# Performance work log

Measured on AMD Instinct MI355X. Metric: run time of the kernel, lower is better.

## Reference

```python
import jax, jax.numpy as jnp
import numpy as np


def setup_inputs() -> dict:
    key = jax.random.key(0)
    ks = jax.random.split(key, 8)
    B, L, C = 128, 196, 2048  # batch, locations (att_size^2), channels
    H, D = 512, 1024          # att_hid_size, decoder hidden_size
    return {
        "att_features": jax.random.normal(ks[0], (B, L, C), dtype=jnp.float32),
        "h": jax.random.normal(ks[1], (B, D), dtype=jnp.float32),
        "Wc": jax.random.normal(ks[2], (L, H), dtype=jnp.float32) * 0.05,
        "bc": jax.random.normal(ks[3], (H,), dtype=jnp.float32) * 0.05,
        "Wh": jax.random.normal(ks[4], (D, H), dtype=jnp.float32) * 0.05,
        "bh": jax.random.normal(ks[5], (H,), dtype=jnp.float32) * 0.05,
        "wa": jax.random.normal(ks[6], (H,), dtype=jnp.float32) * 0.05,
        "ba": jnp.zeros((1,), dtype=jnp.float32),
    }


def reference(att_features, h, Wc, bc, Wh, bh, wa, ba):
    B, L, C = att_features.shape
    # reshape to (B, locations, C) then permute -> (B, C, locations)
    x = jnp.transpose(att_features.reshape(B, L, C), (0, 2, 1))  # (B, C, L)
    ca = jnp.einsum('bcl,lh->bch', x, Wc) + bc                   # channel2att: (B, C, H)
    ph = h @ Wh + bh                                              # h2att: (B, H)
    # alpha_net(tanh(broadcast add)) -> (B, C)
    scores = jnp.einsum('bch,h->bc', jnp.tanh(ca + ph[:, None, :]), wa) + ba[0]
    weights = jax.nn.softmax(scores, axis=1)                      # softmax over channels
    # bmm: (B,1,C) @ (B,C,L) -> (B, L)
    weighted = jnp.einsum('bc,bcl->bl', weights, x)
    return weighted, weights
```

## Files before the change

### kernel.cpp

```cpp
#include <hip/hip_runtime.h>

#define B_   128
#define L_   196
#define C_   2048
#define H_   512
#define D_   1024
#define KP   224
#define CT   256
#define NITER 14

#define SMEM_BYTES (131072 + 4096)

typedef __bf16 bf16x8 __attribute__((ext_vector_type(8)));
typedef float  f32x2  __attribute__((ext_vector_type(2)));
typedef float  f32x4  __attribute__((ext_vector_type(4)));

__device__ __forceinline__ int permc(int c) { return ((c >> 2) & 7) ^ ((c & 2) << 1); }

__global__ __launch_bounds__(256) void k_wc3(const float* __restrict__ Wc, __bf16* __restrict__ wcb3) {
    int grp = blockIdx.x * 256 + threadIdx.x;
    int m  = grp & 15;
    int g  = (grp >> 4) & 3;
    int rb = (grp >> 6) & 31;
    int kk = grp >> 11;
    int h  = rb * 16 + m;
    bf16x8 v;
#pragma unroll
    for (int j = 0; j < 8; ++j) {
        int k = kk * 32 + g * 8 + j;
        v[j] = (k < L_) ? (__bf16)Wc[(size_t)k * H_ + h] : (__bf16)0.0f;
    }
    *(bf16x8*)&wcb3[(size_t)grp * 8] = v;
}

__global__ __launch_bounds__(512) void k_ph(const float* __restrict__ h, const float* __restrict__ Wh,
                                            const float* __restrict__ bh, const float* __restrict__ bc,
                                            float* __restrict__ ph_ws) {
    int b0 = blockIdx.x * 4;
    int t = threadIdx.x;
    __shared__ float hs[4][D_];
    for (int idx = t; idx < 4 * D_; idx += 512)
        hs[idx >> 10][idx & (D_ - 1)] = h[(size_t)(b0 + (idx >> 10)) * D_ + (idx & (D_ - 1))];
    __syncthreads();
    float base = bh[t] + bc[t];
    float a0 = base, a1 = base, a2 = base, a3 = base;
#pragma unroll 8
    for (int d = 0; d < D_; ++d) {
        float wv = Wh[(size_t)d * H_ + t];
        a0 += hs[0][d] * wv; a1 += hs[1][d] * wv; a2 += hs[2][d] * wv; a3 += hs[3][d] * wv;
    }
    ph_ws[(size_t)(b0 + 0) * H_ + t] = a0;
    ph_ws[(size_t)(b0 + 1) * H_ + t] = a1;
    ph_ws[(size_t)(b0 + 2) * H_ + t] = a2;
    ph_ws[(size_t)(b0 + 3) * H_ + t] = a3;
}

__device__ __forceinline__ float fast_tanh(float x) {
    x = fminf(fmaxf(x, -15.f), 15.f);
    float e = __builtin_amdgcn_exp2f(x * 2.8853900817779268f);
    return 1.0f - 2.0f * __builtin_amdgcn_rcpf(e + 1.0f);
}

__global__ __launch_bounds__(512, 2) void k_scores(const float* __restrict__ att, const __bf16* __restrict__ wcb3,
                                                   const float* __restrict__ ph_ws, const float* __restrict__ wa,
                                                   const float* __restrict__ ba, float* __restrict__ scores) {
    extern __shared__ char smem[];
    __bf16* att_s = (__bf16*)smem;
    float*  sred  = (float*)(smem + 131072);

    const int t = threadIdx.x, lane = t & 63, wid = t >> 6;
    const int wm = wid >> 1, wn = wid & 1;
    const int ct = blockIdx.x, b = blockIdx.y;
    const float* attb = att + ((size_t)b * L_) * C_ + ct * CT;

    const int cpr = t & 127, sl = t >> 7;
    const int c0s = cpr * 2;
    const int pmS = permc(c0s);

    const int n_ = lane & 15, g_ = lane >> 4;
    const int crow0 = wn * 128 + n_;
    const int t2 = (n_ & 2) << 1;
    const int qb = crow0 >> 2;

    f32x2 sv[8];
    auto STAGE_LOAD = [&](int kk) {
#pragma unroll
        for (int j = 0; j < 8; ++j) {
            int l = kk * 32 + sl * 8 + j;
            if (l < L_) sv[j] = *(const f32x2*)(attb + (size_t)l * C_ + c0s);
            else { sv[j][0] = 0.f; sv[j][1] = 0.f; }
        }
    };
    auto STAGE_WRITE = [&](int kk) {
        int p = (kk * 4 + sl) ^ pmS;
        bf16x8 r0, r1;
#pragma unroll
        for (int j = 0; j < 8; ++j) { r0[j] = (__bf16)sv[j][0]; r1[j] = (__bf16)sv[j][1]; }
        *(bf16x8*)&att_s[c0s * 256 + p * 8] = r0;
        *(bf16x8*)&att_s[(c0s + 1) * 256 + p * 8] = r1;
    };

    bf16x8 afr[4], afrN[4];
    const __bf16* apA = wcb3 + (size_t)lane * 8;
    auto ALOAD = [&](int it, bf16x8* dst) {
        int hc = (it >= 7) ? 1 : 0;
        int kk = it - hc * 7;
#pragma unroll
        for (int mf = 0; mf < 4; ++mf) {
            int rb = hc * 16 + wm * 4 + mf;
            dst[mf] = *(const bf16x8*)(apA + (size_t)(kk * 32 + rb) * 512);
        }
    };

    ALOAD(0, afr);
    STAGE_LOAD(0);
    STAGE_WRITE(0);
    __syncthreads();

    f32x4 zero4 = {0.f, 0.f, 0.f, 0.f};
    f32x4 acc[4][8];
#pragma unroll
    for (int mf = 0; mf < 4; ++mf)
#pragma unroll
        for (int nf = 0; nf < 8; ++nf) acc[mf][nf] = zero4;
    float spart[8] = {0.f, 0.f, 0.f, 0.f, 0.f, 0.f, 0.f, 0.f};

    for (int it = 0; it < NITER; ++it) {
        const int hc = (it >= 7) ? 1 : 0;
        const int kk = it - hc * 7;

        if (it + 1 < NITER) ALOAD(it + 1, afrN);
        if (it < 6) STAGE_LOAD(it + 1);

        bf16x8 bfr[8];
        const int sb = kk * 4 + g_;
#pragma unroll
        for (int nf = 0; nf < 8; ++nf) {
            int p = sb ^ (((qb + nf * 4) & 7) ^ t2);
            bfr[nf] = *(const bf16x8*)&att_s[(crow0 + nf * 16) * 256 + p * 8];
        }
#pragma unroll
        for (int mf = 0; mf < 4; ++mf)
#pragma unroll
            for (int nf = 0; nf < 8; ++nf)
                acc[mf][nf] = __builtin_amdgcn_mfma_f32_16x16x32_bf16(afr[mf], bfr[nf], acc[mf][nf], 0, 0, 0);

        if (it < 6) STAGE_WRITE(it + 1);

        if (kk == 6) {
            const int rbase = hc * 256 + wm * 64 + g_ * 4;
#pragma unroll
            for (int mf = 0; mf < 4; ++mf) {
                const int row = rbase + mf * 16;
                f32x4 phv = *(const f32x4*)&ph_ws[(size_t)b * H_ + row];
                f32x4 wav = *(const f32x4*)&wa[row];
#pragma unroll
                for (int nf = 0; nf < 8; ++nf) {
                    f32x4 tv = acc[mf][nf];
                    float ss = 0.f;
#pragma unroll
                    for (int r = 0; r < 4; ++r)
                        ss += fast_tanh(tv[r] + phv[r]) * wav[r];
                    spart[nf] += ss;
                    acc[mf][nf] = zero4;
                }
            }
        }

        if (it < 6) __syncthreads();

        if (it + 1 < NITER) {
#pragma unroll
            for (int mf = 0; mf < 4; ++mf) afr[mf] = afrN[mf];
        }
    }

#pragma unroll
    for (int nf = 0; nf < 8; ++nf) {
        spart[nf] += __shfl_xor(spart[nf], 16);
        spart[nf] += __shfl_xor(spart[nf], 32);
    }
    if (g_ == 0) {
#pragma unroll
        for (int nf = 0; nf < 8; ++nf) sred[(wid * 8 + nf) * 16 + n_] = spart[nf];
    }
    __syncthreads();
    if (wid < 2 && g_ == 0) {
        const float ba0 = ba[0];
#pragma unroll
        for (int nf = 0; nf < 8; ++nf) {
            float v = ba0;
#pragma unroll
            for (int wmm = 0; wmm < 4; ++wmm) v += sred[((wmm * 2 + wid) * 8 + nf) * 16 + n_];
            scores[(size_t)b * C_ + ct * CT + wid * 128 + nf * 16 + n_] = v;
        }
    }
}

__global__ __launch_bounds__(512) void k_fused(const float* __restrict__ att, const float* __restrict__ sc,
                                               float* __restrict__ out) {
    __shared__ float w_s[C_];
    __shared__ float red[8], red2[8];
    const int b = blockIdx.y, q = blockIdx.x;
    const int t = threadIdx.x;
    const int lane = t & 63, wid = t >> 6;

    const float* sp = sc + (size_t)b * C_;
    float v[4];
#pragma unroll
    for (int j = 0; j < 4; ++j) v[j] = sp[j * 512 + t];
    float m = fmaxf(fmaxf(v[0], v[1]), fmaxf(v[2], v[3]));
#pragma unroll
    for (int off = 32; off >= 1; off >>= 1) m = fmaxf(m, __shfl_xor(m, off));
    if (lane == 0) red[wid] = m;
    __syncthreads();
#pragma unroll
    for (int w = 0; w < 8; ++w) m = fmaxf(m, red[w]);
    float s = 0.f;
#pragma unroll
    for (int j = 0; j < 4; ++j) {
        v[j] = __builtin_amdgcn_exp2f((v[j] - m) * 1.4426950408889634f);
        s += v[j];
    }
#pragma unroll
    for (int off = 32; off >= 1; off >>= 1) s += __shfl_xor(s, off);
    if (lane == 0) red2[wid] = s;
    __syncthreads();
    s = 0.f;
#pragma unroll
    for (int w = 0; w < 8; ++w) s += red2[w];
    float inv = 1.0f / s;
    float* wout = out + B_ * L_;
#pragma unroll
    for (int j = 0; j < 4; ++j) {
        float wv = v[j] * inv;
        w_s[j * 512 + t] = wv;
        if (q == 0) wout[(size_t)b * C_ + j * 512 + t] = wv;
    }
    __syncthreads();

    for (int l = wid; l < 49; l += 8) {
        int gl = q * 49 + l;
        const float* ap = att + ((size_t)b * L_ + gl) * C_;
        float acc = 0.f;
#pragma unroll
        for (int j = 0; j < 8; ++j) {
            int c = j * 256 + lane * 4;
            f32x4 a4 = *(const f32x4*)(ap + c);
            f32x4 w4 = *(const f32x4*)&w_s[c];
            acc += a4[0] * w4[0] + a4[1] * w4[1] + a4[2] * w4[2] + a4[3] * w4[3];
        }
#pragma unroll
        for (int off = 32; off >= 1; off >>= 1) acc += __shfl_xor(acc, off);
        if (lane == 0) out[(size_t)b * L_ + gl] = acc;
    }
}

extern "C" void kernel_launch(void* const* d_in, const int* in_sizes, int n_in,
                              void* d_out, int out_size, void* d_ws, size_t ws_size,
                              hipStream_t stream) {
    const float* att = (const float*)d_in[0];
    const float* h   = (const float*)d_in[1];
    const float* Wc  = (const float*)d_in[2];
    const float* bc  = (const float*)d_in[3];
    const float* Wh  = (const float*)d_in[4];
    const float* bh  = (const float*)d_in[5];
    const float* wa  = (const float*)d_in[6];
    const float* ba  = (const float*)d_in[7];
    float* out = (float*)d_out;

    float* ph_ws  = (float*)d_ws;
    float* scores = ph_ws + B_ * H_;
    __bf16* wcb3  = (__bf16*)(scores + (size_t)B_ * C_);

    hipFuncSetAttribute((const void*)k_scores, hipFuncAttributeMaxDynamicSharedMemorySize, SMEM_BYTES);

    k_wc3   <<<dim3(56), 256, 0, stream>>>(Wc, wcb3);
    k_ph    <<<dim3(B_ / 4), 512, 0, stream>>>(h, Wh, bh, bc, ph_ws);
    k_scores<<<dim3(C_ / CT, B_), 512, SMEM_BYTES, stream>>>(att, wcb3, ph_ws, wa, ba, scores);
    k_fused <<<dim3(4, B_), 512, 0, stream>>>(att, scores, out);
}
```

Baseline: 454.8 us.

## Halve score tile width, pad LDS rows, merge prep kernels, dual-row weighted sum

The channel tile of the scores kernel drops from 256 to 128 with a padded row stride of 224 bf16 instead of a 256-wide XOR permutation, so LDS use shrinks and launch bounds allow four blocks per CU. The A-fragment double buffer is replaced by loading the next fragments after the MFMAs, the loop is fully unrolled with setprio around the MFMA section, and barriers become a lighter lgkmcnt wait plus s_barrier. The Wc conversion and h2att kernels are merged into one launch, fast_tanh loses its clamp, and the weighted-sum kernel handles two locations per wave iteration for more memory-level parallelism. The narrower tile halves B-fragment reuse per A load and doubles the grid, and without the clamp very large arguments rely on exp2 saturating to inf.

```diff
diff --git a/kernel.cpp b/kernel.cpp
--- a/kernel.cpp
+++ b/kernel.cpp
@@ -5,146 +5,138 @@
 #define C_   2048
 #define H_   512
 #define D_   1024
-#define KP   224
-#define CT   256
+#define CT   128
 #define NITER 14
-
-#define SMEM_BYTES (131072 + 4096)
+#define RSE  224
 
 typedef __bf16 bf16x8 __attribute__((ext_vector_type(8)));
-typedef float  f32x2  __attribute__((ext_vector_type(2)));
 typedef float  f32x4  __attribute__((ext_vector_type(4)));
 
-__device__ __forceinline__ int permc(int c) { return ((c >> 2) & 7) ^ ((c & 2) << 1); }
-
-__global__ __launch_bounds__(256) void k_wc3(const float* __restrict__ Wc, __bf16* __restrict__ wcb3) {
-    int grp = blockIdx.x * 256 + threadIdx.x;
-    int m  = grp & 15;
-    int g  = (grp >> 4) & 3;
-    int rb = (grp >> 6) & 31;
-    int kk = grp >> 11;
-    int h  = rb * 16 + m;
-    bf16x8 v;
-#pragma unroll
-    for (int j = 0; j < 8; ++j) {
-        int k = kk * 32 + g * 8 + j;
-        v[j] = (k < L_) ? (__bf16)Wc[(size_t)k * H_ + h] : (__bf16)0.0f;
-    }
-    *(bf16x8*)&wcb3[(size_t)grp * 8] = v;
-}
-
-__global__ __launch_bounds__(512) void k_ph(const float* __restrict__ h, const float* __restrict__ Wh,
-                                            const float* __restrict__ bh, const float* __restrict__ bc,
-                                            float* __restrict__ ph_ws) {
-    int b0 = blockIdx.x * 4;
-    int t = threadIdx.x;
+__global__ __launch_bounds__(512) void k_prep(const float* __restrict__ Wc, __bf16* __restrict__ wcb3,
+                                              const float* __restrict__ h, const float* __restrict__ Wh,
+                                              const float* __restrict__ bh, const float* __restrict__ bc,
+                                              float* __restrict__ ph_ws) {
     __shared__ float hs[4][D_];
-    for (int idx = t; idx < 4 * D_; idx += 512)
-        hs[idx >> 10][idx & (D_ - 1)] = h[(size_t)(b0 + (idx >> 10)) * D_ + (idx & (D_ - 1))];
-    __syncthreads();
-    float base = bh[t] + bc[t];
-    float a0 = base, a1 = base, a2 = base, a3 = base;
+    const int bid = blockIdx.x, t = threadIdx.x;
+    if (bid < 28) {
+        int grp = bid * 512 + t;
+        int m  = grp & 15;
+        int g  = (grp >> 4) & 3;
+        int rb = (grp >> 6) & 31;
+        int kk = grp >> 11;
+        int hh = rb * 16 + m;
+        bf16x8 v;
+#pragma unroll
+        for (int j = 0; j < 8; ++j) {
+            int k = kk * 32 + g * 8 + j;
+            v[j] = (k < L_) ? (__bf16)Wc[(size_t)k * H_ + hh] : (__bf16)0.0f;
+        }
+        *(bf16x8*)&wcb3[(size_t)grp * 8] = v;
+    } else {
+        int b0 = (bid - 28) * 4;
+        for (int idx = t; idx < 4 * D_; idx += 512)
+            hs[idx >> 10][idx & (D_ - 1)] = h[(size_t)(b0 + (idx >> 10)) * D_ + (idx & (D_ - 1))];
+        __syncthreads();
+        float base = bh[t] + bc[t];
+        float a0 = base, a1 = base, a2 = base, a3 = base;
 #pragma unroll 8
-    for (int d = 0; d < D_; ++d) {
-        float wv = Wh[(size_t)d * H_ + t];
-        a0 += hs[0][d] * wv; a1 += hs[1][d] * wv; a2 += hs[2][d] * wv; a3 += hs[3][d] * wv;
-    }
-    ph_ws[(size_t)(b0 + 0) * H_ + t] = a0;
-    ph_ws[(size_t)(b0 + 1) * H_ + t] = a1;
-    ph_ws[(size_t)(b0 + 2) * H_ + t] = a2;
-    ph_ws[(size_t)(b0 + 3) * H_ + t] = a3;
+        for (int d = 0; d < D_; ++d) {
+            float wv = Wh[(size_t)d * H_ + t];
+            a0 += hs[0][d] * wv; a1 += hs[1][d] * wv; a2 += hs[2][d] * wv; a3 += hs[3][d] * wv;
+        }
+        ph_ws[(size_t)(b0 + 0) * H_ + t] = a0;
+        ph_ws[(size_t)(b0 + 1) * H_ + t] = a1;
+        ph_ws[(size_t)(b0 + 2) * H_ + t] = a2;
+        ph_ws[(size_t)(b0 + 3) * H_ + t] = a3;
+    }
 }
 
 __device__ __forceinline__ float fast_tanh(float x) {
-    x = fminf(fmaxf(x, -15.f), 15.f);
     float e = __builtin_amdgcn_exp2f(x * 2.8853900817779268f);
-    return 1.0f - 2.0f * __builtin_amdgcn_rcpf(e + 1.0f);
-}
-
-__global__ __launch_bounds__(512, 2) void k_scores(const float* __restrict__ att, const __bf16* __restrict__ wcb3,
+    return fmaf(-2.0f, __builtin_amdgcn_rcpf(e + 1.0f), 1.0f);
+}
+
+__device__ __forceinline__ void block_sync_lds() {
+    asm volatile("s_waitcnt lgkmcnt(0)" ::: "memory");
+    __builtin_amdgcn_sched_barrier(0);
+    __builtin_amdgcn_s_barrier();
+    __builtin_amdgcn_sched_barrier(0);
+}
+
+__global__ __launch_bounds__(512, 4) void k_scores(const float* __restrict__ att, const __bf16* __restrict__ wcb3,
                                                    const float* __restrict__ ph_ws, const float* __restrict__ wa,
                                                    const float* __restrict__ ba, float* __restrict__ scores) {
-    extern __shared__ char smem[];
-    __bf16* att_s = (__bf16*)smem;
-    float*  sred  = (float*)(smem + 131072);
+    __shared__ __bf16 att_s[CT * RSE];
+    __shared__ float  sred[8][4][16];
 
     const int t = threadIdx.x, lane = t & 63, wid = t >> 6;
     const int wm = wid >> 1, wn = wid & 1;
     const int ct = blockIdx.x, b = blockIdx.y;
     const float* attb = att + ((size_t)b * L_) * C_ + ct * CT;
 
-    const int cpr = t & 127, sl = t >> 7;
-    const int c0s = cpr * 2;
-    const int pmS = permc(c0s);
+    const int sc = t & 127, sl = t >> 7;
+    const int spdst = sc * RSE + (sl ^ ((sc >> 1) & 3)) * 8;
 
     const int n_ = lane & 15, g_ = lane >> 4;
-    const int crow0 = wn * 128 + n_;
-    const int t2 = (n_ & 2) << 1;
-    const int qb = crow0 >> 2;
-
-    f32x2 sv[8];
+    const int bbase = (wn * 64 + n_) * RSE + (g_ ^ ((n_ >> 1) & 3)) * 8;
+
+    const __bf16* apA = wcb3 + (size_t)lane * 8;
+
+    float sv[8];
+    bf16x8 afr[4];
+
     auto STAGE_LOAD = [&](int kk) {
 #pragma unroll
         for (int j = 0; j < 8; ++j) {
             int l = kk * 32 + sl * 8 + j;
-            if (l < L_) sv[j] = *(const f32x2*)(attb + (size_t)l * C_ + c0s);
-            else { sv[j][0] = 0.f; sv[j][1] = 0.f; }
+            sv[j] = (l < L_) ? attb[(size_t)l * C_ + sc] : 0.0f;
         }
     };
     auto STAGE_WRITE = [&](int kk) {
-        int p = (kk * 4 + sl) ^ pmS;
-        bf16x8 r0, r1;
-#pragma unroll
-        for (int j = 0; j < 8; ++j) { r0[j] = (__bf16)sv[j][0]; r1[j] = (__bf16)sv[j][1]; }
-        *(bf16x8*)&att_s[c0s * 256 + p * 8] = r0;
-        *(bf16x8*)&att_s[(c0s + 1) * 256 + p * 8] = r1;
+        bf16x8 r;
+#pragma unroll
+        for (int j = 0; j < 8; ++j) r[j] = (__bf16)sv[j];
+        *(bf16x8*)&att_s[spdst + kk * 32] = r;
     };
-
-    bf16x8 afr[4], afrN[4];
-    const __bf16* apA = wcb3 + (size_t)lane * 8;
-    auto ALOAD = [&](int it, bf16x8* dst) {
+    auto ALOAD = [&](int it) {
         int hc = (it >= 7) ? 1 : 0;
         int kk = it - hc * 7;
 #pragma unroll
-        for (int mf = 0; mf < 4; ++mf) {
-            int rb = hc * 16 + wm * 4 + mf;
-            dst[mf] = *(const bf16x8*)(apA + (size_t)(kk * 32 + rb) * 512);
-        }
+        for (int mf = 0; mf < 4; ++mf)
+            afr[mf] = *(const bf16x8*)(apA + (size_t)(kk * 32 + hc * 16 + wm * 4 + mf) * 512);
     };
 
-    ALOAD(0, afr);
     STAGE_LOAD(0);
+    ALOAD(0);
     STAGE_WRITE(0);
-    __syncthreads();
+    block_sync_lds();
 
     f32x4 zero4 = {0.f, 0.f, 0.f, 0.f};
-    f32x4 acc[4][8];
+    f32x4 acc[4][4];
 #pragma unroll
     for (int mf = 0; mf < 4; ++mf)
 #pragma unroll
-        for (int nf = 0; nf < 8; ++nf) acc[mf][nf] = zero4;
-    float spart[8] = {0.f, 0.f, 0.f, 0.f, 0.f, 0.f, 0.f, 0.f};
-
+        for (int nf = 0; nf < 4; ++nf) acc[mf][nf] = zero4;
+    float spart[4] = {0.f, 0.f, 0.f, 0.f};
+
+#pragma unroll
     for (int it = 0; it < NITER; ++it) {
         const int hc = (it >= 7) ? 1 : 0;
         const int kk = it - hc * 7;
 
-        if (it + 1 < NITER) ALOAD(it + 1, afrN);
         if (it < 6) STAGE_LOAD(it + 1);
 
-        bf16x8 bfr[8];
-        const int sb = kk * 4 + g_;
-#pragma unroll
-        for (int nf = 0; nf < 8; ++nf) {
-            int p = sb ^ (((qb + nf * 4) & 7) ^ t2);
-            bfr[nf] = *(const bf16x8*)&att_s[(crow0 + nf * 16) * 256 + p * 8];
-        }
-#pragma unroll
-        for (int mf = 0; mf < 4; ++mf)
-#pragma unroll
-            for (int nf = 0; nf < 8; ++nf)
-                acc[mf][nf] = __builtin_amdgcn_mfma_f32_16x16x32_bf16(afr[mf], bfr[nf], acc[mf][nf], 0, 0, 0);
-
+        __builtin_amdgcn_s_setprio(1);
+#pragma unroll
+        for (int nf = 0; nf < 4; ++nf) {
+            bf16x8 bfr = *(const bf16x8*)&att_s[bbase + nf * 16 * RSE + kk * 32];
+#pragma unroll
+            for (int mf = 0; mf < 4; ++mf)
+                acc[mf][nf] = __builtin_amdgcn_mfma_f32_16x16x32_bf16(afr[mf], bfr, acc[mf][nf], 0, 0, 0);
+        }
+        __builtin_amdgcn_s_setprio(0);
+
+        if (it + 1 < NITER) ALOAD(it + 1);
         if (it < 6) STAGE_WRITE(it + 1);
 
         if (kk == 6) {
@@ -155,7 +147,7 @@
                 f32x4 phv = *(const f32x4*)&ph_ws[(size_t)b * H_ + row];
                 f32x4 wav = *(const f32x4*)&wa[row];
 #pragma unroll
-                for (int nf = 0; nf < 8; ++nf) {
+                for (int nf = 0; nf < 4; ++nf) {
                     f32x4 tv = acc[mf][nf];
                     float ss = 0.f;
 #pragma unroll
@@ -167,32 +159,27 @@
             }
         }
 
-        if (it < 6) __syncthreads();
-
-        if (it + 1 < NITER) {
-#pragma unroll
-            for (int mf = 0; mf < 4; ++mf) afr[mf] = afrN[mf];
-        }
-    }
-
-#pragma unroll
-    for (int nf = 0; nf < 8; ++nf) {
+        if (it < 6) block_sync_lds();
+    }
+
+#pragma unroll
+    for (int nf = 0; nf < 4; ++nf) {
         spart[nf] += __shfl_xor(spart[nf], 16);
         spart[nf] += __shfl_xor(spart[nf], 32);
     }
     if (g_ == 0) {
 #pragma unroll
-        for (int nf = 0; nf < 8; ++nf) sred[(wid * 8 + nf) * 16 + n_] = spart[nf];
+        for (int nf = 0; nf < 4; ++nf) sred[wid][nf][n_] = spart[nf];
     }
     __syncthreads();
     if (wid < 2 && g_ == 0) {
         const float ba0 = ba[0];
 #pragma unroll
-        for (int nf = 0; nf < 8; ++nf) {
+        for (int nf = 0; nf < 4; ++nf) {
             float v = ba0;
 #pragma unroll
-            for (int wmm = 0; wmm < 4; ++wmm) v += sred[((wmm * 2 + wid) * 8 + nf) * 16 + n_];
-            scores[(size_t)b * C_ + ct * CT + wid * 128 + nf * 16 + n_] = v;
+            for (int wmm = 0; wmm < 4; ++wmm) v += sred[wmm * 2 + wid][nf][n_];
+            scores[(size_t)b * C_ + ct * CT + wid * 64 + nf * 16 + n_] = v;
         }
     }
 }
@@ -239,20 +226,30 @@
     }
     __syncthreads();
 
-    for (int l = wid; l < 49; l += 8) {
-        int gl = q * 49 + l;
-        const float* ap = att + ((size_t)b * L_ + gl) * C_;
-        float acc = 0.f;
+    for (int l0 = wid; l0 < 49; l0 += 16) {
+        const int l1 = l0 + 8;
+        const bool has1 = (l1 < 49);
+        const float* ap0 = att + ((size_t)b * L_ + (q * 49 + l0)) * C_;
+        const float* ap1 = att + ((size_t)b * L_ + (q * 49 + (has1 ? l1 : l0))) * C_;
+        float a0 = 0.f, a1 = 0.f;
 #pragma unroll
         for (int j = 0; j < 8; ++j) {
             int c = j * 256 + lane * 4;
-            f32x4 a4 = *(const f32x4*)(ap + c);
+            f32x4 x0 = *(const f32x4*)(ap0 + c);
+            f32x4 x1 = *(const f32x4*)(ap1 + c);
             f32x4 w4 = *(const f32x4*)&w_s[c];
-            acc += a4[0] * w4[0] + a4[1] * w4[1] + a4[2] * w4[2] + a4[3] * w4[3];
-        }
-#pragma unroll
-        for (int off = 32; off >= 1; off >>= 1) acc += __shfl_xor(acc, off);
-        if (lane == 0) out[(size_t)b * L_ + gl] = acc;
+            a0 += x0[0] * w4[0] + x0[1] * w4[1] + x0[2] * w4[2] + x0[3] * w4[3];
+            a1 += x1[0] * w4[0] + x1[1] * w4[1] + x1[2] * w4[2] + x1[3] * w4[3];
+        }
+#pragma unroll
+        for (int off = 32; off >= 1; off >>= 1) {
+            a0 += __shfl_xor(a0, off);
+            a1 += __shfl_xor(a1, off);
+        }
+        if (lane == 0) {
+            out[(size_t)b * L_ + q * 49 + l0] = a0;
+            if (has1) out[(size_t)b * L_ + q * 49 + l1] = a1;
+        }
     }
 }
 
@@ -273,10 +270,7 @@
     float* scores = ph_ws + B_ * H_;
     __bf16* wcb3  = (__bf16*)(scores + (size_t)B_ * C_);
 
-    hipFuncSetAttribute((const void*)k_scores, hipFuncAttributeMaxDynamicSharedMemorySize, SMEM_BYTES);
-
-    k_wc3   <<<dim3(56), 256, 0, stream>>>(Wc, wcb3);
-    k_ph    <<<dim3(B_ / 4), 512, 0, stream>>>(h, Wh, bh, bc, ph_ws);
-    k_scores<<<dim3(C_ / CT, B_), 512, SMEM_BYTES, stream>>>(att, wcb3, ph_ws, wa, ba, scores);
+    k_prep  <<<dim3(60), 512, 0, stream>>>(Wc, wcb3, h, Wh, bh, bc, ph_ws);
+    k_scores<<<dim3(C_ / CT, B_), 512, 0, stream>>>(att, wcb3, ph_ws, wa, ba, scores);
     k_fused <<<dim3(4, B_), 512, 0, stream>>>(att, scores, out);
 }
```

Measured after the change: 440.4 us. 3.2% less time.
